# Kernel tuning notes

Measured on AMD Instinct MI355X. Metric: run time of the kernel, lower is better.

Reference implementation:

```python
import jax, jax.numpy as jnp
import numpy as np

ALPHA = 0.05
NUM_LAYERS = 2


def setup_inputs() -> dict:
    key = jax.random.key(0)
    k1, k2, k3, k4, k5 = jax.random.split(key, 5)
    N, F, C, E = 100000, 64, 40, 1600000
    x = jax.random.normal(k1, (N, F), dtype=jnp.float32)
    edge_attr = jax.random.uniform(k2, (E,), dtype=jnp.float32)
    lin_w = jax.random.normal(k3, (F, C), dtype=jnp.float32) * (1.0 / np.sqrt(F))
    lin_b = jax.random.normal(k4, (C,), dtype=jnp.float32) * 0.01
    edge_index = jax.random.randint(k5, (2, E), 0, N, dtype=jnp.int64)
    return {"x": x, "edge_attr": edge_attr, "lin_w": lin_w, "lin_b": lin_b,
            "edge_index": edge_index}


def reference(x, edge_attr, lin_w, lin_b, edge_index):
    N = x.shape[0]
    row, col = edge_index[0], edge_index[1]
    # symmetric GCN normalization with edge weights
    deg = jax.ops.segment_sum(edge_attr, col, num_segments=N)  # [N]
    dis = jnp.where(deg > 0, jax.lax.rsqrt(jnp.maximum(deg, 1e-12)), 0.0)
    norm = dis[row] * edge_attr * dis[col]  # [E]

    def conv(h):
        # gather source features, scale, scatter-add to targets
        return jax.ops.segment_sum(norm[:, None] * h[row], col, num_segments=N)

    x_input = ALPHA * x
    scale = (1.0 - ALPHA) / NUM_LAYERS
    h = x
    acc = jnp.zeros_like(x)
    for _ in range(NUM_LAYERS):
        h = conv(h)
        acc = acc + scale * h
    out = acc + x_input
    logits = out @ lin_w + lin_b
    return jax.nn.log_softmax(logits, axis=1)
```

## Files before the change

### kernel.cpp

```cpp
#include <hip/hip_runtime.h>
#include <math.h>
#include <string.h>


#define ALPHA  0.05f
#define SCALE  0.475f
#define FDIM   64
#define CDIM   40
#define NPAD   131072
#define CHUNK  8192
#define BCAP   10240
#define SRCMASK 0x1FFFFu

__device__ __forceinline__ unsigned short f2bf(float f) {
    unsigned u = __float_as_uint(f);
    unsigned r = (u + 0x7FFFu + ((u >> 16) & 1u)) >> 16;
    return (unsigned short)r;
}
__device__ __forceinline__ float bfLo(unsigned u) { return __uint_as_float(u << 16); }
__device__ __forceinline__ float bfHi(unsigned u) { return __uint_as_float(u & 0xffff0000u); }
__device__ __forceinline__ float wUnpack(unsigned v) {
    return __uint_as_float((v >> 17) << 16);
}

__global__ __launch_bounds__(256) void zero_alloc(int* __restrict__ alloc) {
    alloc[threadIdx.x] = 0;
}

__global__ __launch_bounds__(1024) void part_scatter(
        const int* __restrict__ row, const int* __restrict__ col,
        const float* __restrict__ ea, int* __restrict__ alloc,
        int2* __restrict__ ppay, int E) {
    __shared__ unsigned h[256];
    __shared__ unsigned offs[256];
    int tid = threadIdx.x, blk = blockIdx.x;
    if (tid < 256) h[tid] = 0;
    __syncthreads();
    int base = blk * CHUNK;
    int end  = min(base + CHUNK, E);
    for (int e = base + tid; e < end; e += 1024)
        atomicAdd(&h[col[e] >> 9], 1u);
    __syncthreads();
    if (tid < 256) {
        unsigned hc = h[tid];
        unsigned r = hc ? (unsigned)atomicAdd(&alloc[tid], (int)hc) : 0u;
        offs[tid] = (unsigned)(tid * BCAP) + r;
    }
    __syncthreads();
    for (int e = base + tid; e < end; e += 1024) {
        int c = col[e];
        int bin = c >> 9;
        unsigned p = atomicAdd(&offs[bin], 1u);
        if (p < (unsigned)((bin + 1) * BCAP))
            ppay[p] = make_int2(row[e] | ((c & 511) << 20), __float_as_int(ea[e]));
    }
}

__global__ __launch_bounds__(256) void bucket_csr(
        const int2* __restrict__ ppay, const int* __restrict__ alloc,
        int* __restrict__ start, unsigned* __restrict__ csr,
        float* __restrict__ dis, int N) {
    __shared__ unsigned cnt8[512][8];
    __shared__ unsigned ps[256], exc[512];
    __shared__ float sdeg[512];
    __shared__ int sAll[256];
    int tid = threadIdx.x, k = blockIdx.x;

    int myCnt = min(alloc[tid], BCAP);
    sAll[tid] = myCnt;
    __syncthreads();
    for (int off = 1; off < 256; off <<= 1) {
        int t = (tid >= off) ? sAll[tid - off] : 0;
        __syncthreads();
        sAll[tid] += t;
        __syncthreads();
    }
    int cnt = min(alloc[k], BCAP);
    int e0  = sAll[k] - cnt;
    const int2* src = ppay + (size_t)k * BCAP;

    for (int i = tid; i < 4096; i += 256) ((unsigned*)cnt8)[i] = 0;
    sdeg[tid] = 0.0f; sdeg[tid + 256] = 0.0f;
    __syncthreads();

    for (int j = tid; j < cnt; j += 256) {
        int2 pay = src[j];
        int c = (pay.x >> 20) & 511;
        atomicAdd(&cnt8[c][(pay.x & 0xFFFFF) >> 14], 1u);
        atomicAdd(&sdeg[c], __int_as_float(pay.y));
    }
    __syncthreads();

    int c0 = 2 * tid, c1 = 2 * tid + 1;
    unsigned t0 = 0, t1 = 0;
    #pragma unroll
    for (int o = 0; o < 8; ++o) { t0 += cnt8[c0][o]; t1 += cnt8[c1][o]; }
    unsigned pair = t0 + t1;
    ps[tid] = pair;
    __syncthreads();
    for (int off = 1; off < 256; off <<= 1) {
        unsigned t = (tid >= off) ? ps[tid - off] : 0;
        __syncthreads();
        ps[tid] += t;
        __syncthreads();
    }
    unsigned pexc = ps[tid] - pair;
    exc[c0] = pexc;
    exc[c1] = pexc + t0;
    unsigned b = pexc;
    #pragma unroll
    for (int o = 0; o < 8; ++o) { unsigned t = cnt8[c0][o]; cnt8[c0][o] = b; b += t; }
    b = pexc + t0;
    #pragma unroll
    for (int o = 0; o < 8; ++o) { unsigned t = cnt8[c1][o]; cnt8[c1][o] = b; b += t; }
    __syncthreads();

    #pragma unroll
    for (int i = tid; i < 512; i += 256) {
        int g = k * 512 + i;
        if (g <= N) start[g] = e0 + (int)exc[i];
        if (g < N) {
            float d = sdeg[i];
            dis[g] = (d > 0.0f) ? rsqrtf(fmaxf(d, 1e-12f)) : 0.0f;
        }
    }

    for (int j = tid; j < cnt; j += 256) {
        int2 pay = src[j];
        int c    = (pay.x >> 20) & 511;
        int srcn = pay.x & 0xFFFFF;
        unsigned p = atomicAdd(&cnt8[c][srcn >> 14], 1u);
        unsigned wbf = (unsigned)f2bf(__int_as_float(pay.y));
        csr[e0 + p] = (unsigned)srcn | (wbf << 17);
    }
}

__global__ void csr_scale_kernel(unsigned* __restrict__ csr,
                                 const float* __restrict__ dis, int E) {
    int stride = gridDim.x * blockDim.x;
    for (int e = blockIdx.x * blockDim.x + threadIdx.x; e < E; e += stride) {
        unsigned v = csr[e];
        unsigned src = v & SRCMASK;
        float w = wUnpack(v) * dis[src];
        csr[e] = src | ((unsigned)f2bf(w) << 17);
    }
}

__global__ __launch_bounds__(256) void lin_kernel(
        const float* __restrict__ x, const float* __restrict__ W,
        unsigned* __restrict__ ybf, int N) {
    __shared__ float sWt[CDIM][FDIM + 4];
    for (int i = threadIdx.x; i < FDIM * CDIM; i += 256) {
        int k = i / CDIM, c = i - k * CDIM;
        sWt[c][k] = W[i];
    }
    __syncthreads();

    int t = threadIdx.x;
    int node = blockIdx.x * 64 + (t >> 2);
    if (node >= N) return;
    int cs = (t & 3) * 10;

    float acc[10];
    #pragma unroll
    for (int i = 0; i < 10; ++i) acc[i] = 0.0f;

    const float4* xr = (const float4*)(x + (size_t)node * FDIM);
    #pragma unroll
    for (int k4 = 0; k4 < FDIM / 4; ++k4) {
        float4 v = xr[k4];
        #pragma unroll
        for (int i = 0; i < 10; ++i) {
            const float4 w = *(const float4*)&sWt[cs + i][k4 * 4];
            acc[i] = fmaf(v.x, w.x, fmaf(v.y, w.y, fmaf(v.z, w.z, fmaf(v.w, w.w, acc[i]))));
        }
    }

    unsigned* yr = ybf + (size_t)node * (CDIM / 2) + (t & 3) * 5;
    #pragma unroll
    for (int k = 0; k < 5; ++k)
        yr[k] = (unsigned)f2bf(acc[2 * k]) | ((unsigned)f2bf(acc[2 * k + 1]) << 16);
}

__global__ __launch_bounds__(256) void spmv_kernel(
        const unsigned* __restrict__ gin, const int* __restrict__ start,
        const unsigned* __restrict__ csr, const float* __restrict__ dis,
        unsigned* __restrict__ gout, int N) {
    int lane = threadIdx.x & 63;
    int wid  = threadIdx.x >> 6;
    int grp  = lane / 10;
    int grel = lane - grp * 10;
    int node = blockIdx.x * 24 + wid * 6 + grp;
    bool act = (grp < 6) && (node < N);

    int e0 = 0, e1 = 0;
    if (act) { e0 = start[node]; e1 = start[node + 1]; }
    const uint2* gin2 = (const uint2*)gin;

    float a0 = 0, a1 = 0, a2 = 0, a3 = 0;
    float b0 = 0, b1 = 0, b2 = 0, b3 = 0;
    int j = e0;
    for (; j + 7 < e1; j += 8) {
        unsigned v0 = csr[j],     v1 = csr[j + 1], v2 = csr[j + 2], v3 = csr[j + 3];
        unsigned v4 = csr[j + 4], v5 = csr[j + 5], v6 = csr[j + 6], v7 = csr[j + 7];
        uint2 u0 = gin2[(size_t)(v0 & SRCMASK) * 10 + grel];
        uint2 u1 = gin2[(size_t)(v1 & SRCMASK) * 10 + grel];
        uint2 u2 = gin2[(size_t)(v2 & SRCMASK) * 10 + grel];
        uint2 u3 = gin2[(size_t)(v3 & SRCMASK) * 10 + grel];
        uint2 u4 = gin2[(size_t)(v4 & SRCMASK) * 10 + grel];
        uint2 u5 = gin2[(size_t)(v5 & SRCMASK) * 10 + grel];
        uint2 u6 = gin2[(size_t)(v6 & SRCMASK) * 10 + grel];
        uint2 u7 = gin2[(size_t)(v7 & SRCMASK) * 10 + grel];
        float w0 = wUnpack(v0), w1 = wUnpack(v1), w2 = wUnpack(v2), w3 = wUnpack(v3);
        float w4 = wUnpack(v4), w5 = wUnpack(v5), w6 = wUnpack(v6), w7 = wUnpack(v7);
        a0 = fmaf(w0, bfLo(u0.x), a0); a1 = fmaf(w0, bfHi(u0.x), a1);
        a2 = fmaf(w0, bfLo(u0.y), a2); a3 = fmaf(w0, bfHi(u0.y), a3);
        b0 = fmaf(w1, bfLo(u1.x), b0); b1 = fmaf(w1, bfHi(u1.x), b1);
        b2 = fmaf(w1, bfLo(u1.y), b2); b3 = fmaf(w1, bfHi(u1.y), b3);
        a0 = fmaf(w2, bfLo(u2.x), a0); a1 = fmaf(w2, bfHi(u2.x), a1);
        a2 = fmaf(w2, bfLo(u2.y), a2); a3 = fmaf(w2, bfHi(u2.y), a3);
        b0 = fmaf(w3, bfLo(u3.x), b0); b1 = fmaf(w3, bfHi(u3.x), b1);
        b2 = fmaf(w3, bfLo(u3.y), b2); b3 = fmaf(w3, bfHi(u3.y), b3);
        a0 = fmaf(w4, bfLo(u4.x), a0); a1 = fmaf(w4, bfHi(u4.x), a1);
        a2 = fmaf(w4, bfLo(u4.y), a2); a3 = fmaf(w4, bfHi(u4.y), a3);
        b0 = fmaf(w5, bfLo(u5.x), b0); b1 = fmaf(w5, bfHi(u5.x), b1);
        b2 = fmaf(w5, bfLo(u5.y), b2); b3 = fmaf(w5, bfHi(u5.y), b3);
        a0 = fmaf(w6, bfLo(u6.x), a0); a1 = fmaf(w6, bfHi(u6.x), a1);
        a2 = fmaf(w6, bfLo(u6.y), a2); a3 = fmaf(w6, bfHi(u6.y), a3);
        b0 = fmaf(w7, bfLo(u7.x), b0); b1 = fmaf(w7, bfHi(u7.x), b1);
        b2 = fmaf(w7, bfLo(u7.y), b2); b3 = fmaf(w7, bfHi(u7.y), b3);
    }
    for (; j < e1; ++j) {
        unsigned v = csr[j];
        uint2 u = gin2[(size_t)(v & SRCMASK) * 10 + grel];
        float w = wUnpack(v);
        a0 = fmaf(w, bfLo(u.x), a0); a1 = fmaf(w, bfHi(u.x), a1);
        a2 = fmaf(w, bfLo(u.y), a2); a3 = fmaf(w, bfHi(u.y), a3);
    }
    if (act) {
        float dn = dis[node];
        float f0 = dn * (a0 + b0), f1 = dn * (a1 + b1);
        float f2 = dn * (a2 + b2), f3 = dn * (a3 + b3);
        uint2 o;
        o.x = (unsigned)f2bf(f0) | ((unsigned)f2bf(f1) << 16);
        o.y = (unsigned)f2bf(f2) | ((unsigned)f2bf(f3) << 16);
        ((uint2*)gout)[(size_t)node * 10 + grel] = o;
    }
}

__global__ __launch_bounds__(256) void spmv_final_kernel(
        const unsigned* __restrict__ g1, const unsigned* __restrict__ y,
        const float* __restrict__ bias, const int* __restrict__ start,
        const unsigned* __restrict__ csr, const float* __restrict__ dis,
        float* __restrict__ out, int N) {
    int lane = threadIdx.x & 63;
    int wid  = threadIdx.x >> 6;
    int grp  = lane / 10;
    int grel = lane - grp * 10;
    int node = blockIdx.x * 24 + wid * 6 + grp;
    bool act = (grp < 6) && (node < N);

    int e0 = 0, e1 = 0;
    if (act) { e0 = start[node]; e1 = start[node + 1]; }
    const uint2* g12 = (const uint2*)g1;

    float a0 = 0, a1 = 0, a2 = 0, a3 = 0;
    float b0 = 0, b1 = 0, b2 = 0, b3 = 0;
    int j = e0;
    for (; j + 7 < e1; j += 8) {
        unsigned v0 = csr[j],     v1 = csr[j + 1], v2 = csr[j + 2], v3 = csr[j + 3];
        unsigned v4 = csr[j + 4], v5 = csr[j + 5], v6 = csr[j + 6], v7 = csr[j + 7];
        uint2 u0 = g12[(size_t)(v0 & SRCMASK) * 10 + grel];
        uint2 u1 = g12[(size_t)(v1 & SRCMASK) * 10 + grel];
        uint2 u2 = g12[(size_t)(v2 & SRCMASK) * 10 + grel];
        uint2 u3 = g12[(size_t)(v3 & SRCMASK) * 10 + grel];
        uint2 u4 = g12[(size_t)(v4 & SRCMASK) * 10 + grel];
        uint2 u5 = g12[(size_t)(v5 & SRCMASK) * 10 + grel];
        uint2 u6 = g12[(size_t)(v6 & SRCMASK) * 10 + grel];
        uint2 u7 = g12[(size_t)(v7 & SRCMASK) * 10 + grel];
        float w0 = wUnpack(v0), w1 = wUnpack(v1), w2 = wUnpack(v2), w3 = wUnpack(v3);
        float w4 = wUnpack(v4), w5 = wUnpack(v5), w6 = wUnpack(v6), w7 = wUnpack(v7);
        a0 = fmaf(w0, bfLo(u0.x), a0); a1 = fmaf(w0, bfHi(u0.x), a1);
        a2 = fmaf(w0, bfLo(u0.y), a2); a3 = fmaf(w0, bfHi(u0.y), a3);
        b0 = fmaf(w1, bfLo(u1.x), b0); b1 = fmaf(w1, bfHi(u1.x), b1);
        b2 = fmaf(w1, bfLo(u1.y), b2); b3 = fmaf(w1, bfHi(u1.y), b3);
        a0 = fmaf(w2, bfLo(u2.x), a0); a1 = fmaf(w2, bfHi(u2.x), a1);
        a2 = fmaf(w2, bfLo(u2.y), a2); a3 = fmaf(w2, bfHi(u2.y), a3);
        b0 = fmaf(w3, bfLo(u3.x), b0); b1 = fmaf(w3, bfHi(u3.x), b1);
        b2 = fmaf(w3, bfLo(u3.y), b2); b3 = fmaf(w3, bfHi(u3.y), b3);
        a0 = fmaf(w4, bfLo(u4.x), a0); a1 = fmaf(w4, bfHi(u4.x), a1);
        a2 = fmaf(w4, bfLo(u4.y), a2); a3 = fmaf(w4, bfHi(u4.y), a3);
        b0 = fmaf(w5, bfLo(u5.x), b0); b1 = fmaf(w5, bfHi(u5.x), b1);
        b2 = fmaf(w5, bfLo(u5.y), b2); b3 = fmaf(w5, bfHi(u5.y), b3);
        a0 = fmaf(w6, bfLo(u6.x), a0); a1 = fmaf(w6, bfHi(u6.x), a1);
        a2 = fmaf(w6, bfLo(u6.y), a2); a3 = fmaf(w6, bfHi(u6.y), a3);
        b0 = fmaf(w7, bfLo(u7.x), b0); b1 = fmaf(w7, bfHi(u7.x), b1);
        b2 = fmaf(w7, bfLo(u7.y), b2); b3 = fmaf(w7, bfHi(u7.y), b3);
    }
    for (; j < e1; ++j) {
        unsigned v = csr[j];
        uint2 u = g12[(size_t)(v & SRCMASK) * 10 + grel];
        float w = wUnpack(v);
        a0 = fmaf(w, bfLo(u.x), a0); a1 = fmaf(w, bfHi(u.x), a1);
        a2 = fmaf(w, bfLo(u.y), a2); a3 = fmaf(w, bfHi(u.y), a3);
    }

    float l0 = 0, l1 = 0, l2 = 0, l3 = 0;
    if (act) {
        float dn = dis[node];
        float g20 = dn * (a0 + b0), g21 = dn * (a1 + b1);
        float g22 = dn * (a2 + b2), g23 = dn * (a3 + b3);
        uint2 yu = ((const uint2*)y)[(size_t)node * 10 + grel];
        uint2 gu = g12[(size_t)node * 10 + grel];
        float4 bv = *(const float4*)&bias[4 * grel];
        l0 = fmaf(ALPHA, bfLo(yu.x), fmaf(SCALE, bfLo(gu.x) + g20, bv.x));
        l1 = fmaf(ALPHA, bfHi(yu.x), fmaf(SCALE, bfHi(gu.x) + g21, bv.y));
        l2 = fmaf(ALPHA, bfLo(yu.y), fmaf(SCALE, bfLo(gu.y) + g22, bv.z));
        l3 = fmaf(ALPHA, bfHi(yu.y), fmaf(SCALE, bfHi(gu.y) + g23, bv.w));
    }

    float m = act ? fmaxf(fmaxf(l0, l1), fmaxf(l2, l3)) : -INFINITY;
    #pragma unroll
    for (int off = 8; off; off >>= 1) {
        float o = __shfl(m, lane + off);
        if (grel + off < 10) m = fmaxf(m, o);
    }
    m = __shfl(m, grp * 10);

    float ex = act ? (expf(l0 - m) + expf(l1 - m) + expf(l2 - m) + expf(l3 - m)) : 0.0f;
    #pragma unroll
    for (int off = 8; off; off >>= 1) {
        float o = __shfl(ex, lane + off);
        if (grel + off < 10) ex += o;
    }
    ex = __shfl(ex, grp * 10);

    if (act) {
        float lse = m + logf(ex);
        float2 oA, oB;
        oA.x = l0 - lse; oA.y = l1 - lse;
        oB.x = l2 - lse; oB.y = l3 - lse;
        double dA, dB;
        memcpy(&dA, &oA, 8);
        memcpy(&dB, &oB, 8);
        double* p = (double*)&out[(size_t)node * CDIM + 4 * grel];
        __builtin_nontemporal_store(dA, p);
        __builtin_nontemporal_store(dB, p + 1);
    }
}

extern "C" void kernel_launch(void* const* d_in, const int* in_sizes, int n_in,
                              void* d_out, int out_size, void* d_ws, size_t ws_size,
                              hipStream_t stream) {
    const float* x  = (const float*)d_in[0];
    const float* ea = (const float*)d_in[1];
    const float* W  = (const float*)d_in[2];
    const float* b  = (const float*)d_in[3];
    const int*   ei = (const int*)d_in[4];

    const int N = in_sizes[0] / FDIM;
    const int E = in_sizes[1];
    const int* row = ei;
    const int* col = ei + E;

    const int NBLK = (E + CHUNK - 1) / CHUNK;

    int*   startp = (int*)d_ws;
    float* dis    = (float*)(startp + NPAD);
    int*   alloc  = (int*)(dis + NPAD);
    int2*  ppay   = (int2*)(alloc + 1024);
    unsigned* csr = (unsigned*)(ppay + 256 * BCAP);
    unsigned* g1bf = csr + E;
    unsigned* ybf  = (unsigned*)ppay;

    zero_alloc  <<<1, 256, 0, stream>>>(alloc);
    part_scatter<<<NBLK, 1024, 0, stream>>>(row, col, ea, alloc, ppay, E);
    bucket_csr  <<<256, 256, 0, stream>>>(ppay, alloc, startp, csr, dis, N);
    csr_scale_kernel<<<2048, 256, 0, stream>>>(csr, dis, E);
    lin_kernel  <<<(N + 63) / 64, 256, 0, stream>>>(x, W, ybf, N);

    int spmv_blocks = (N + 23) / 24;
    spmv_kernel      <<<spmv_blocks, 256, 0, stream>>>(ybf, startp, csr, dis, g1bf, N);
    spmv_final_kernel<<<spmv_blocks, 256, 0, stream>>>(g1bf, ybf, b, startp, csr, dis,
                                                       (float*)d_out, N);
}
```

Baseline: 146.2 us.

## Fold source-side degree scaling into node features instead of rescaling CSR weights

Drops the separate csr_scale pass that read and rewrote every edge weight multiplied by dis[src]. The source-side normalization is now applied per node: lin_kernel writes a dis-prescaled copy z1 of the projected features, and spmv_kernel writes both g1 and a dis-prescaled z2 for the next layer. This trades a pass over 1.6M edges for extra per-node bf16 writes of two feature arrays. It also changes where bf16 rounding happens in the normalization.

```diff
diff --git a/kernel.cpp b/kernel.cpp
--- a/kernel.cpp
+++ b/kernel.cpp
@@ -135,20 +135,10 @@
     }
 }
 
-__global__ void csr_scale_kernel(unsigned* __restrict__ csr,
-                                 const float* __restrict__ dis, int E) {
-    int stride = gridDim.x * blockDim.x;
-    for (int e = blockIdx.x * blockDim.x + threadIdx.x; e < E; e += stride) {
-        unsigned v = csr[e];
-        unsigned src = v & SRCMASK;
-        float w = wUnpack(v) * dis[src];
-        csr[e] = src | ((unsigned)f2bf(w) << 17);
-    }
-}
-
 __global__ __launch_bounds__(256) void lin_kernel(
         const float* __restrict__ x, const float* __restrict__ W,
-        unsigned* __restrict__ ybf, int N) {
+        const float* __restrict__ dis,
+        unsigned* __restrict__ ybf, unsigned* __restrict__ z1, int N) {
     __shared__ float sWt[CDIM][FDIM + 4];
     for (int i = threadIdx.x; i < FDIM * CDIM; i += 256) {
         int k = i / CDIM, c = i - k * CDIM;
@@ -176,16 +166,20 @@
         }
     }
 
-    unsigned* yr = ybf + (size_t)node * (CDIM / 2) + (t & 3) * 5;
-    #pragma unroll
-    for (int k = 0; k < 5; ++k)
+    float dn = dis[node];
+    unsigned* yr = ybf + (size_t)node * 20 + (t & 3) * 5;
+    unsigned* zr = z1  + (size_t)node * 20 + (t & 3) * 5;
+    #pragma unroll
+    for (int k = 0; k < 5; ++k) {
         yr[k] = (unsigned)f2bf(acc[2 * k]) | ((unsigned)f2bf(acc[2 * k + 1]) << 16);
+        zr[k] = (unsigned)f2bf(dn * acc[2 * k]) | ((unsigned)f2bf(dn * acc[2 * k + 1]) << 16);
+    }
 }
 
 __global__ __launch_bounds__(256) void spmv_kernel(
-        const unsigned* __restrict__ gin, const int* __restrict__ start,
+        const unsigned* __restrict__ z1, const int* __restrict__ start,
         const unsigned* __restrict__ csr, const float* __restrict__ dis,
-        unsigned* __restrict__ gout, int N) {
+        unsigned* __restrict__ g1, unsigned* __restrict__ z2, int N) {
     int lane = threadIdx.x & 63;
     int wid  = threadIdx.x >> 6;
     int grp  = lane / 10;
@@ -195,7 +189,7 @@
 
     int e0 = 0, e1 = 0;
     if (act) { e0 = start[node]; e1 = start[node + 1]; }
-    const uint2* gin2 = (const uint2*)gin;
+    const uint2* gin2 = (const uint2*)z1;
 
     float a0 = 0, a1 = 0, a2 = 0, a3 = 0;
     float b0 = 0, b1 = 0, b2 = 0, b3 = 0;
@@ -239,20 +233,23 @@
     }
     if (act) {
         float dn = dis[node];
-        float f0 = dn * (a0 + b0), f1 = dn * (a1 + b1);
-        float f2 = dn * (a2 + b2), f3 = dn * (a3 + b3);
-        uint2 o;
-        o.x = (unsigned)f2bf(f0) | ((unsigned)f2bf(f1) << 16);
-        o.y = (unsigned)f2bf(f2) | ((unsigned)f2bf(f3) << 16);
-        ((uint2*)gout)[(size_t)node * 10 + grel] = o;
+        float t0 = a0 + b0, t1 = a1 + b1, t2 = a2 + b2, t3 = a3 + b3;
+        float gg0 = dn * t0, gg1 = dn * t1, gg2 = dn * t2, gg3 = dn * t3;
+        uint2 og, oz;
+        og.x = (unsigned)f2bf(gg0) | ((unsigned)f2bf(gg1) << 16);
+        og.y = (unsigned)f2bf(gg2) | ((unsigned)f2bf(gg3) << 16);
+        oz.x = (unsigned)f2bf(dn * gg0) | ((unsigned)f2bf(dn * gg1) << 16);
+        oz.y = (unsigned)f2bf(dn * gg2) | ((unsigned)f2bf(dn * gg3) << 16);
+        ((uint2*)g1)[(size_t)node * 10 + grel] = og;
+        ((uint2*)z2)[(size_t)node * 10 + grel] = oz;
     }
 }
 
 __global__ __launch_bounds__(256) void spmv_final_kernel(
-        const unsigned* __restrict__ g1, const unsigned* __restrict__ y,
-        const float* __restrict__ bias, const int* __restrict__ start,
-        const unsigned* __restrict__ csr, const float* __restrict__ dis,
-        float* __restrict__ out, int N) {
+        const unsigned* __restrict__ z2, const unsigned* __restrict__ g1,
+        const unsigned* __restrict__ y, const float* __restrict__ bias,
+        const int* __restrict__ start, const unsigned* __restrict__ csr,
+        const float* __restrict__ dis, float* __restrict__ out, int N) {
     int lane = threadIdx.x & 63;
     int wid  = threadIdx.x >> 6;
     int grp  = lane / 10;
@@ -262,7 +259,7 @@
 
     int e0 = 0, e1 = 0;
     if (act) { e0 = start[node]; e1 = start[node + 1]; }
-    const uint2* g12 = (const uint2*)g1;
+    const uint2* g22 = (const uint2*)z2;
 
     float a0 = 0, a1 = 0, a2 = 0, a3 = 0;
     float b0 = 0, b1 = 0, b2 = 0, b3 = 0;
@@ -270,14 +267,14 @@
     for (; j + 7 < e1; j += 8) {
         unsigned v0 = csr[j],     v1 = csr[j + 1], v2 = csr[j + 2], v3 = csr[j + 3];
         unsigned v4 = csr[j + 4], v5 = csr[j + 5], v6 = csr[j + 6], v7 = csr[j + 7];
-        uint2 u0 = g12[(size_t)(v0 & SRCMASK) * 10 + grel];
-        uint2 u1 = g12[(size_t)(v1 & SRCMASK) * 10 + grel];
-        uint2 u2 = g12[(size_t)(v2 & SRCMASK) * 10 + grel];
-        uint2 u3 = g12[(size_t)(v3 & SRCMASK) * 10 + grel];
-        uint2 u4 = g12[(size_t)(v4 & SRCMASK) * 10 + grel];
-        uint2 u5 = g12[(size_t)(v5 & SRCMASK) * 10 + grel];
-        uint2 u6 = g12[(size_t)(v6 & SRCMASK) * 10 + grel];
-        uint2 u7 = g12[(size_t)(v7 & SRCMASK) * 10 + grel];
+        uint2 u0 = g22[(size_t)(v0 & SRCMASK) * 10 + grel];
+        uint2 u1 = g22[(size_t)(v1 & SRCMASK) * 10 + grel];
+        uint2 u2 = g22[(size_t)(v2 & SRCMASK) * 10 + grel];
+        uint2 u3 = g22[(size_t)(v3 & SRCMASK) * 10 + grel];
+        uint2 u4 = g22[(size_t)(v4 & SRCMASK) * 10 + grel];
+        uint2 u5 = g22[(size_t)(v5 & SRCMASK) * 10 + grel];
+        uint2 u6 = g22[(size_t)(v6 & SRCMASK) * 10 + grel];
+        uint2 u7 = g22[(size_t)(v7 & SRCMASK) * 10 + grel];
         float w0 = wUnpack(v0), w1 = wUnpack(v1), w2 = wUnpack(v2), w3 = wUnpack(v3);
         float w4 = wUnpack(v4), w5 = wUnpack(v5), w6 = wUnpack(v6), w7 = wUnpack(v7);
         a0 = fmaf(w0, bfLo(u0.x), a0); a1 = fmaf(w0, bfHi(u0.x), a1);
@@ -299,7 +296,7 @@
     }
     for (; j < e1; ++j) {
         unsigned v = csr[j];
-        uint2 u = g12[(size_t)(v & SRCMASK) * 10 + grel];
+        uint2 u = g22[(size_t)(v & SRCMASK) * 10 + grel];
         float w = wUnpack(v);
         a0 = fmaf(w, bfLo(u.x), a0); a1 = fmaf(w, bfHi(u.x), a1);
         a2 = fmaf(w, bfLo(u.y), a2); a3 = fmaf(w, bfHi(u.y), a3);
@@ -309,13 +306,13 @@
     if (act) {
         float dn = dis[node];
         float g20 = dn * (a0 + b0), g21 = dn * (a1 + b1);
-        float g22 = dn * (a2 + b2), g23 = dn * (a3 + b3);
+        float g22v = dn * (a2 + b2), g23 = dn * (a3 + b3);
         uint2 yu = ((const uint2*)y)[(size_t)node * 10 + grel];
-        uint2 gu = g12[(size_t)node * 10 + grel];
+        uint2 gu = ((const uint2*)g1)[(size_t)node * 10 + grel];
         float4 bv = *(const float4*)&bias[4 * grel];
         l0 = fmaf(ALPHA, bfLo(yu.x), fmaf(SCALE, bfLo(gu.x) + g20, bv.x));
         l1 = fmaf(ALPHA, bfHi(yu.x), fmaf(SCALE, bfHi(gu.x) + g21, bv.y));
-        l2 = fmaf(ALPHA, bfLo(yu.y), fmaf(SCALE, bfLo(gu.y) + g22, bv.z));
+        l2 = fmaf(ALPHA, bfLo(yu.y), fmaf(SCALE, bfLo(gu.y) + g22v, bv.z));
         l3 = fmaf(ALPHA, bfHi(yu.y), fmaf(SCALE, bfHi(gu.y) + g23, bv.w));
     }
 
@@ -371,16 +368,17 @@
     int2*  ppay   = (int2*)(alloc + 1024);
     unsigned* csr = (unsigned*)(ppay + 256 * BCAP);
     unsigned* g1bf = csr + E;
+    unsigned* z2bf = g1bf + (size_t)N * 20;
     unsigned* ybf  = (unsigned*)ppay;
+    unsigned* z1bf = ybf + (size_t)N * 20;
 
     zero_alloc  <<<1, 256, 0, stream>>>(alloc);
     part_scatter<<<NBLK, 1024, 0, stream>>>(row, col, ea, alloc, ppay, E);
     bucket_csr  <<<256, 256, 0, stream>>>(ppay, alloc, startp, csr, dis, N);
-    csr_scale_kernel<<<2048, 256, 0, stream>>>(csr, dis, E);
-    lin_kernel  <<<(N + 63) / 64, 256, 0, stream>>>(x, W, ybf, N);
+    lin_kernel  <<<(N + 63) / 64, 256, 0, stream>>>(x, W, dis, ybf, z1bf, N);
 
     int spmv_blocks = (N + 23) / 24;
-    spmv_kernel      <<<spmv_blocks, 256, 0, stream>>>(ybf, startp, csr, dis, g1bf, N);
-    spmv_final_kernel<<<spmv_blocks, 256, 0, stream>>>(g1bf, ybf, b, startp, csr, dis,
+    spmv_kernel      <<<spmv_blocks, 256, 0, stream>>>(z1bf, startp, csr, dis, g1bf, z2bf, N);
+    spmv_final_kernel<<<spmv_blocks, 256, 0, stream>>>(z2bf, g1bf, ybf, b, startp, csr, dis,
                                                        (float*)d_out, N);
 }
```

New measurement: 139.4 us. -4.6%, faster.
